# Optimization experiments

Measured on AMD Instinct MI355X. Metric: run time of the kernel, lower is better.

## Reference

```python
import jax, jax.numpy as jnp
import numpy as np

THR = 1.0
ALPHA = 5.0
C = 0.4
TAU_U = 20.0
DT = 1.0

def slayer(x):
    # SE-adlif SLAYER surrogate: c*alpha / (2*exp(alpha*|x|))
    return C * ALPHA / (2.0 * jnp.exp(jnp.abs(x) * ALPHA))

def setup_inputs() -> dict:
    key = jax.random.key(0)
    k1, k2, k3 = jax.random.split(key, 3)
    B, T, IN, OUT = 64, 1000, 512, 512
    x = jax.random.normal(k1, (B, T, IN), dtype=jnp.float32)
    lim = 1.0 / np.sqrt(IN)
    weight = jax.random.uniform(k2, (OUT, IN), minval=-lim, maxval=lim, dtype=jnp.float32)
    bias = jnp.zeros((OUT,), jnp.float32)
    # orthogonal init for recurrent weights
    recurrent = jnp.linalg.qr(jax.random.normal(k3, (OUT, OUT), dtype=jnp.float32))[0].astype(jnp.float32)
    # fixed tau trainer: decay = exp(-dt/tau)
    decay = jnp.full((OUT,), np.exp(-DT / TAU_U), dtype=jnp.float32)
    return {"input_tensor": x, "weight": weight, "bias": bias, "recurrent": recurrent, "decay": decay}

def reference(input_tensor, weight, bias, recurrent, decay):
    B = input_tensor.shape[0]
    OUT = weight.shape[0]
    sg = jax.lax.stop_gradient
    # precompute input-driven current for all timesteps: [B, T, OUT]
    cur = jnp.einsum('bti,oi->bto', input_tensor, weight) + bias
    v0 = jnp.zeros((B, OUT), jnp.float32)
    z0 = jnp.zeros((B, OUT), jnp.float32)

    def step(carry, c_t):
        v_tm1, z_tm1 = carry
        v_tm1 = v_tm1 * (1.0 - sg(z_tm1))  # detached reset
        soma = c_t + z_tm1 @ recurrent.T
        v_t = decay * v_tm1 + (1.0 - decay) * soma
        v_thr = v_t - THR
        hv = jnp.where(v_thr >= 0, 1.0, 0.0).astype(v_thr.dtype)
        # straight-through: value = heaviside, grad = SLAYER surrogate
        z_t = sg(hv) + (v_thr - sg(v_thr)) * sg(slayer(v_thr))
        return (v_t, z_t), (v_t, z_t)

    _, (vs, zs) = jax.lax.scan(step, (v0, z0), jnp.swapaxes(cur, 0, 1))
    vs = jnp.swapaxes(vs, 0, 1)  # [B, T, OUT]
    zs = jnp.swapaxes(zs, 0, 1)
    v_full = jnp.concatenate([v0[:, None], vs], axis=1)  # [B, T+1, OUT]
    z_full = jnp.concatenate([z0[:, None], zs], axis=1)
    states = jnp.stack([v_full, z_full], axis=0)  # [2, B, T+1, OUT]
    outputs = zs  # [B, T, OUT]
    return outputs, states
```

## Files before the change

kernel.cpp:

```cpp
#include <hip/hip_runtime.h>
#include <hip/hip_bf16.h>

#define SV_OFF 32768000
#define SZ_OFF 65568768
#define TC 125
#define NC 8

typedef __attribute__((ext_vector_type(8))) short bf16x8;
typedef __attribute__((ext_vector_type(4))) float f32x4;

__device__ __forceinline__ unsigned short f2bf(float f) {
  union { float f; unsigned u; } x; x.f = f;
  unsigned r = x.u + 0x7fffu + ((x.u >> 16) & 1u);
  return (unsigned short)(r >> 16);
}

__device__ __forceinline__ void gl_lds16(const void* g, void* l) {
  __builtin_amdgcn_global_load_lds(
      (const __attribute__((address_space(1))) unsigned int*)g,
      (__attribute__((address_space(3))) unsigned int*)l, 16, 0, 0);
}

__global__ __launch_bounds__(256) void prep(const float* __restrict__ W,
                                            const float* __restrict__ R,
                                            unsigned short* __restrict__ Wb,
                                            float* __restrict__ RT,
                                            int* __restrict__ flags) {
  const int idx = blockIdx.x * 256 + threadIdx.x;
  if (idx < 512 * 512) {
    Wb[idx] = f2bf(W[idx]);
    const int j = idx >> 9;
    const int o = idx & 511;
    RT[idx] = R[o * 512 + j];
  }
  if (idx < 64) flags[idx] = 0;
}

__global__ __launch_bounds__(256) void cvt_x(const float* __restrict__ x,
                                             unsigned short* __restrict__ xb) {
  const size_t i = ((size_t)blockIdx.x * 256 + threadIdx.x) * 8;
  const float4 a = *(const float4*)(x + i);
  const float4 b = *(const float4*)(x + i + 4);
  bf16x8 h;
  h[0] = (short)f2bf(a.x); h[1] = (short)f2bf(a.y);
  h[2] = (short)f2bf(a.z); h[3] = (short)f2bf(a.w);
  h[4] = (short)f2bf(b.x); h[5] = (short)f2bf(b.y);
  h[6] = (short)f2bf(b.z); h[7] = (short)f2bf(b.w);
  *(bf16x8*)(xb + i) = h;
}

__global__ __launch_bounds__(256, 2) void gemm_cur(
    const unsigned short* __restrict__ Ab,
    const unsigned short* __restrict__ Wb,
    const float* __restrict__ bias,
    float* __restrict__ C) {
  __shared__ unsigned short As[128][32];
  __shared__ unsigned short Bs[128][32];
  const int tid = threadIdx.x;
  const int bn = blockIdx.x * 128;
  const int bm = blockIdx.y * 128;
  const int wave = tid >> 6;
  const int lane = tid & 63;
  const int lr = lane & 15;
  const int lq = lane >> 4;
  const int mh = (wave & 1) * 64;
  const int nh = (wave >> 1) * 64;

  f32x4 acc[4][4] = {};

  const int lo0 = tid * 16;
  const int row0 = lo0 >> 6;
  const int colb = lo0 & 63;
  const size_t abase = (size_t)(bm + row0) * 1024 + colb;
  const size_t bbase = (size_t)(bn + row0) * 1024 + colb;

  for (int kk = 0; kk < 16; ++kk) {
    const size_t koff = (size_t)kk * 64;
    __syncthreads();
    gl_lds16((const char*)Ab + abase + koff,            (char*)(&As[0][0]) + lo0);
    gl_lds16((const char*)Ab + abase + 65536 + koff,    (char*)(&As[0][0]) + lo0 + 4096);
    gl_lds16((const char*)Wb + bbase + koff,            (char*)(&Bs[0][0]) + lo0);
    gl_lds16((const char*)Wb + bbase + 65536 + koff,    (char*)(&Bs[0][0]) + lo0 + 4096);
    __syncthreads();
    bf16x8 af[4], bfr[4];
#pragma unroll
    for (int i = 0; i < 4; ++i)
      af[i] = *(const bf16x8*)(&As[mh + i * 16 + lr][lq * 8]);
#pragma unroll
    for (int j = 0; j < 4; ++j)
      bfr[j] = *(const bf16x8*)(&Bs[nh + j * 16 + lr][lq * 8]);
#pragma unroll
    for (int i = 0; i < 4; ++i)
#pragma unroll
      for (int j = 0; j < 4; ++j)
        acc[i][j] = __builtin_amdgcn_mfma_f32_16x16x32_bf16(af[i], bfr[j], acc[i][j], 0, 0, 0);
  }
#pragma unroll
  for (int j = 0; j < 4; ++j) {
    const int col = bn + nh + j * 16 + lr;
    const float bv = bias[col];
#pragma unroll
    for (int i = 0; i < 4; ++i) {
      const int r0 = bm + mh + i * 16 + lq * 4;
#pragma unroll
      for (int r = 0; r < 4; ++r)
        C[(size_t)(r0 + r) * 512 + col] = acc[i][j][r] + bv;
    }
  }
}

__global__ __launch_bounds__(256) void chunk_sums(const float* __restrict__ cur,
                                                  const float* __restrict__ decay,
                                                  float* __restrict__ S) {
  const int gt = blockIdx.x * 256 + threadIdx.x;
  const int o = gt & 511;
  const int j = (gt >> 9) & (NC - 1);
  const int b = gt >> 12;
  const float d = decay[o];
  const float om = 1.0f - d;
  const size_t base = (size_t)b * 512000 + (size_t)(j * TC) * 512 + o;
  float nb[8];
#pragma unroll
  for (int u = 0; u < 8; ++u) nb[u] = cur[base + (size_t)u * 512];
  float s = 0.f;
#pragma unroll 8
  for (int k = 0; k < TC; ++k) {
    const float c = nb[k & 7];
    if (k < TC - 8) nb[k & 7] = cur[base + (size_t)(k + 8) * 512];
    s = d * s + om * c;
  }
  S[gt] = s;
}

__global__ __launch_bounds__(256) void chunk_scan(const float* __restrict__ cur,
                                                  const float* __restrict__ decay,
                                                  const float* __restrict__ S,
                                                  float* __restrict__ out,
                                                  int* __restrict__ flags) {
  const int gt = blockIdx.x * 256 + threadIdx.x;
  const int o = gt & 511;
  const int j = (gt >> 9) & (NC - 1);
  const int b = gt >> 12;
  const float d = decay[o];
  const float om = 1.0f - d;
  const size_t ci = (size_t)b * 512000 + (size_t)(j * TC) * 512 + o;
  const size_t svb = (size_t)b * 512512 + (size_t)(j * TC) * 512 + o;
  float* __restrict__ sv = out + SV_OFF;
  float* __restrict__ sz = out + SZ_OFF;
  if (j == 0) {
    __builtin_nontemporal_store(0.f, &sv[svb]);
    __builtin_nontemporal_store(0.f, &sz[svb]);
  }
  float v = 0.f;
  if (j > 0) {
    const float dTC = powf(d, (float)TC);
    const int sb = (b << 12) + o;
    for (int jj = 0; jj < j; ++jj) v = dTC * v + S[sb + (jj << 9)];
  }
  int fl = 0;
  float nb[8];
#pragma unroll
  for (int u = 0; u < 8; ++u) nb[u] = cur[ci + (size_t)u * 512];
#pragma unroll 8
  for (int k = 0; k < TC; ++k) {
    const float c = nb[k & 7];
    if (k < TC - 8) nb[k & 7] = cur[ci + (size_t)(k + 8) * 512];
    v = d * v + om * c;
    const float z = (v >= 1.0f) ? 1.0f : 0.0f;
    fl |= (v >= 1.0f);
    const size_t row = (size_t)k * 512;
    __builtin_nontemporal_store(z, &out[ci + row]);
    __builtin_nontemporal_store(v, &sv[svb + row + 512]);
    __builtin_nontemporal_store(z, &sz[svb + row + 512]);
  }
  if (fl) atomicOr(flags + b, 1);
}

__global__ __launch_bounds__(512) void scan_fix(const float* __restrict__ cur,
                                                const float* __restrict__ decay,
                                                const float* __restrict__ RT,
                                                float* __restrict__ out,
                                                const int* __restrict__ flags) {
  const int b = blockIdx.x;
  if (flags[b] == 0) return;
  const int o = threadIdx.x;
  __shared__ int cnt;
  __shared__ int list[512];
  const float d = decay[o];
  const float om = 1.f - d;
  float v = 0.f, z = 0.f;
  const size_t ci = (size_t)b * 512000 + o;
  const size_t svb = (size_t)b * 512512 + o;
  float* __restrict__ sv = out + SV_OFF;
  float* __restrict__ sz = out + SZ_OFF;
  sv[svb] = 0.f;
  sz[svb] = 0.f;
  if (o == 0) cnt = 0;
  __syncthreads();
  for (int t = 0; t < 1000; ++t) {
    float soma = cur[ci + (size_t)t * 512];
    const int n = cnt;
    for (int i = 0; i < n; ++i) soma += RT[(size_t)list[i] * 512 + o];
    v = d * (v * (1.f - z)) + om * soma;
    z = (v >= 1.0f) ? 1.0f : 0.0f;
    out[ci + (size_t)t * 512] = z;
    sv[svb + (size_t)(t + 1) * 512] = v;
    sz[svb + (size_t)(t + 1) * 512] = z;
    __syncthreads();
    if (o == 0) cnt = 0;
    __syncthreads();
    if (z != 0.f) { const int p = atomicAdd(&cnt, 1); list[p] = o; }
    __syncthreads();
  }
}

extern "C" void kernel_launch(void* const* d_in, const int* in_sizes, int n_in,
                              void* d_out, int out_size, void* d_ws, size_t ws_size,
                              hipStream_t stream) {
  (void)in_sizes; (void)n_in; (void)out_size; (void)ws_size;
  const float* x     = (const float*)d_in[0];
  const float* W     = (const float*)d_in[1];
  const float* bias  = (const float*)d_in[2];
  const float* R     = (const float*)d_in[3];
  const float* decay = (const float*)d_in[4];
  float* out = (float*)d_out;

  char* ws = (char*)d_ws;
  float* cur          = (float*)ws;
  unsigned short* Wb  = (unsigned short*)(ws + 131072000);
  float* RT           = (float*)(ws + 131596288);
  int* flags          = (int*)(ws + 132644864);
  float* S            = (float*)(ws + 132648960);

  unsigned short* xb = (unsigned short*)(out + SV_OFF);

  prep<<<1024, 256, 0, stream>>>(W, R, Wb, RT, flags);
  cvt_x<<<16000, 256, 0, stream>>>(x, xb);
  gemm_cur<<<dim3(4, 500), 256, 0, stream>>>(xb, Wb, bias, cur);
  chunk_sums<<<1024, 256, 0, stream>>>(cur, decay, S);
  chunk_scan<<<1024, 256, 0, stream>>>(cur, decay, S, out, flags);
  scan_fix<<<64, 512, 0, stream>>>(cur, decay, RT, out, flags);
}
```

Before: 603.3 us.

## Fuse input GEMM with leaky integration scan to eliminate current buffer

Replaces the separate GEMM, chunk-sum and chunk-scan kernels with one kernel. Each block owns one batch row and 64 outputs, walks time in 128-step tiles with double-buffered LDS staging, and stages the accumulators in swizzled shared memory. 64 threads then run the serial leaky scan straight from that tile. This removes the full fp32 current tensor round trip through global memory. The fallback spike-recurrence kernel now recomputes the input projection in fp32 from x and W, and the recurrent transpose is dropped. The costs are that most threads sit idle during the serial scan and the fallback path becomes much more expensive if it is triggered.

```diff
diff --git a/kernel.cpp b/kernel.cpp
--- a/kernel.cpp
+++ b/kernel.cpp
@@ -1,10 +1,7 @@
 #include <hip/hip_runtime.h>
-#include <hip/hip_bf16.h>
 
 #define SV_OFF 32768000
 #define SZ_OFF 65568768
-#define TC 125
-#define NC 8
 
 typedef __attribute__((ext_vector_type(8))) short bf16x8;
 typedef __attribute__((ext_vector_type(4))) float f32x4;
@@ -22,17 +19,10 @@
 }
 
 __global__ __launch_bounds__(256) void prep(const float* __restrict__ W,
-                                            const float* __restrict__ R,
                                             unsigned short* __restrict__ Wb,
-                                            float* __restrict__ RT,
                                             int* __restrict__ flags) {
   const int idx = blockIdx.x * 256 + threadIdx.x;
-  if (idx < 512 * 512) {
-    Wb[idx] = f2bf(W[idx]);
-    const int j = idx >> 9;
-    const int o = idx & 511;
-    RT[idx] = R[o * 512 + j];
-  }
+  if (idx < 512 * 512) Wb[idx] = f2bf(W[idx]);
   if (idx < 64) flags[idx] = 0;
 }
 
@@ -49,147 +39,128 @@
   *(bf16x8*)(xb + i) = h;
 }
 
-__global__ __launch_bounds__(256, 2) void gemm_cur(
+__global__ __launch_bounds__(256, 2) void fused(
     const unsigned short* __restrict__ Ab,
     const unsigned short* __restrict__ Wb,
     const float* __restrict__ bias,
-    float* __restrict__ C) {
-  __shared__ unsigned short As[128][32];
-  __shared__ unsigned short Bs[128][32];
-  const int tid = threadIdx.x;
-  const int bn = blockIdx.x * 128;
-  const int bm = blockIdx.y * 128;
+    const float* __restrict__ decay,
+    float* __restrict__ out,
+    int* __restrict__ flags) {
+  __shared__ unsigned short As[2][128][32];
+  __shared__ unsigned short Bs[2][64][32];
+  __shared__ float cs[128][64];
+
+  const int b    = blockIdx.x;
+  const int o0   = blockIdx.y * 64;
+  const int tid  = threadIdx.x;
   const int wave = tid >> 6;
   const int lane = tid & 63;
   const int lr = lane & 15;
   const int lq = lane >> 4;
-  const int mh = (wave & 1) * 64;
-  const int nh = (wave >> 1) * 64;
-
-  f32x4 acc[4][4] = {};
-
-  const int lo0 = tid * 16;
-  const int row0 = lo0 >> 6;
-  const int colb = lo0 & 63;
-  const size_t abase = (size_t)(bm + row0) * 1024 + colb;
-  const size_t bbase = (size_t)(bn + row0) * 1024 + colb;
-
-  for (int kk = 0; kk < 16; ++kk) {
-    const size_t koff = (size_t)kk * 64;
-    __syncthreads();
-    gl_lds16((const char*)Ab + abase + koff,            (char*)(&As[0][0]) + lo0);
-    gl_lds16((const char*)Ab + abase + 65536 + koff,    (char*)(&As[0][0]) + lo0 + 4096);
-    gl_lds16((const char*)Wb + bbase + koff,            (char*)(&Bs[0][0]) + lo0);
-    gl_lds16((const char*)Wb + bbase + 65536 + koff,    (char*)(&Bs[0][0]) + lo0 + 4096);
-    __syncthreads();
-    bf16x8 af[4], bfr[4];
+  const int wr = wave >> 1;
+  const int wc = wave & 1;
+
+  const int arow = tid >> 2;
+  const int acb  = (tid & 3) * 16;
+  const char* abase = (const char*)Ab + (size_t)b * 1000 * 1024;
+  const char* bbase = (const char*)Wb + (size_t)o0 * 1024;
+
+#define STAGE(pp, t0s, kks) do {                                                   \
+    const int _kb = (kks) * 64 + acb;                                              \
+    gl_lds16(abase + (size_t)((t0s) + arow) * 1024 + _kb,                          \
+             (char*)&As[pp][0][0] + tid * 16);                                     \
+    gl_lds16(abase + (size_t)((t0s) + 64 + arow) * 1024 + _kb,                     \
+             (char*)&As[pp][0][0] + tid * 16 + 4096);                              \
+    gl_lds16(bbase + (size_t)arow * 1024 + _kb,                                    \
+             (char*)&Bs[pp][0][0] + tid * 16);                                     \
+  } while (0)
+
+  float v = 0.f, d = 0.f, om = 0.f, bv = 0.f;
+  int fl = 0;
+  if (tid < 64) {
+    d  = decay[o0 + tid];
+    om = 1.f - d;
+    bv = bias[o0 + tid];
+    __builtin_nontemporal_store(0.f, out + SV_OFF + (size_t)b * 512512 + o0 + tid);
+    __builtin_nontemporal_store(0.f, out + SZ_OFF + (size_t)b * 512512 + o0 + tid);
+  }
+
+  int p = 0;
+  STAGE(0, 0, 0);
+  for (int tile = 0; tile < 8; ++tile) {
+    const int t0 = tile * 128;
+    f32x4 acc[4][2] = {};
+    for (int kk = 0; kk < 16; ++kk) {
+      __syncthreads();
+      if (kk < 15)       STAGE(p ^ 1, t0, kk + 1);
+      else if (tile < 7) STAGE(p ^ 1, t0 + 128, 0);
+      bf16x8 af[4], bf[2];
+#pragma unroll
+      for (int i = 0; i < 4; ++i)
+        af[i] = *(const bf16x8*)(&As[p][wr * 64 + i * 16 + lr][lq * 8]);
+#pragma unroll
+      for (int j = 0; j < 2; ++j)
+        bf[j] = *(const bf16x8*)(&Bs[p][wc * 32 + j * 16 + lr][lq * 8]);
+#pragma unroll
+      for (int i = 0; i < 4; ++i)
+#pragma unroll
+        for (int j = 0; j < 2; ++j)
+          acc[i][j] = __builtin_amdgcn_mfma_f32_16x16x32_bf16(af[i], bf[j], acc[i][j], 0, 0, 0);
+      p ^= 1;
+    }
 #pragma unroll
     for (int i = 0; i < 4; ++i)
-      af[i] = *(const bf16x8*)(&As[mh + i * 16 + lr][lq * 8]);
-#pragma unroll
-    for (int j = 0; j < 4; ++j)
-      bfr[j] = *(const bf16x8*)(&Bs[nh + j * 16 + lr][lq * 8]);
-#pragma unroll
-    for (int i = 0; i < 4; ++i)
-#pragma unroll
-      for (int j = 0; j < 4; ++j)
-        acc[i][j] = __builtin_amdgcn_mfma_f32_16x16x32_bf16(af[i], bfr[j], acc[i][j], 0, 0, 0);
-  }
-#pragma unroll
-  for (int j = 0; j < 4; ++j) {
-    const int col = bn + nh + j * 16 + lr;
-    const float bv = bias[col];
-#pragma unroll
-    for (int i = 0; i < 4; ++i) {
-      const int r0 = bm + mh + i * 16 + lq * 4;
-#pragma unroll
-      for (int r = 0; r < 4; ++r)
-        C[(size_t)(r0 + r) * 512 + col] = acc[i][j][r] + bv;
+#pragma unroll
+      for (int j = 0; j < 2; ++j) {
+        const int tb = wr * 64 + i * 16 + lq * 4;
+        const int cc = (wc * 32 + j * 16 + lr) ^ ((lq & 1) << 4);
+#pragma unroll
+        for (int r = 0; r < 4; ++r) cs[tb + r][cc] = acc[i][j][r];
+      }
+    __syncthreads();
+    if (tid < 64) {
+      const int tmax = (tile == 7) ? 104 : 128;
+      float* zp = out + ((size_t)b * 1000 + t0) * 512 + o0 + tid;
+      float* vp = out + SV_OFF + ((size_t)b * 1001 + t0 + 1) * 512 + o0 + tid;
+      float* sp = out + SZ_OFF + ((size_t)b * 1001 + t0 + 1) * 512 + o0 + tid;
+      for (int t = 0; t < tmax; t += 4) {
+        const int cc = tid ^ (((t >> 2) & 1) << 4);
+        float c4[4];
+#pragma unroll
+        for (int u = 0; u < 4; ++u) c4[u] = cs[t + u][cc];
+#pragma unroll
+        for (int u = 0; u < 4; ++u) {
+          v = d * v + om * (c4[u] + bv);
+          const float z = (v >= 1.0f) ? 1.0f : 0.0f;
+          fl |= (v >= 1.0f);
+          __builtin_nontemporal_store(z, zp + (size_t)(t + u) * 512);
+          __builtin_nontemporal_store(v, vp + (size_t)(t + u) * 512);
+          __builtin_nontemporal_store(z, sp + (size_t)(t + u) * 512);
+        }
+      }
     }
   }
-}
-
-__global__ __launch_bounds__(256) void chunk_sums(const float* __restrict__ cur,
-                                                  const float* __restrict__ decay,
-                                                  float* __restrict__ S) {
-  const int gt = blockIdx.x * 256 + threadIdx.x;
-  const int o = gt & 511;
-  const int j = (gt >> 9) & (NC - 1);
-  const int b = gt >> 12;
-  const float d = decay[o];
-  const float om = 1.0f - d;
-  const size_t base = (size_t)b * 512000 + (size_t)(j * TC) * 512 + o;
-  float nb[8];
-#pragma unroll
-  for (int u = 0; u < 8; ++u) nb[u] = cur[base + (size_t)u * 512];
-  float s = 0.f;
-#pragma unroll 8
-  for (int k = 0; k < TC; ++k) {
-    const float c = nb[k & 7];
-    if (k < TC - 8) nb[k & 7] = cur[base + (size_t)(k + 8) * 512];
-    s = d * s + om * c;
-  }
-  S[gt] = s;
-}
-
-__global__ __launch_bounds__(256) void chunk_scan(const float* __restrict__ cur,
-                                                  const float* __restrict__ decay,
-                                                  const float* __restrict__ S,
-                                                  float* __restrict__ out,
-                                                  int* __restrict__ flags) {
-  const int gt = blockIdx.x * 256 + threadIdx.x;
-  const int o = gt & 511;
-  const int j = (gt >> 9) & (NC - 1);
-  const int b = gt >> 12;
-  const float d = decay[o];
-  const float om = 1.0f - d;
-  const size_t ci = (size_t)b * 512000 + (size_t)(j * TC) * 512 + o;
-  const size_t svb = (size_t)b * 512512 + (size_t)(j * TC) * 512 + o;
-  float* __restrict__ sv = out + SV_OFF;
-  float* __restrict__ sz = out + SZ_OFF;
-  if (j == 0) {
-    __builtin_nontemporal_store(0.f, &sv[svb]);
-    __builtin_nontemporal_store(0.f, &sz[svb]);
-  }
-  float v = 0.f;
-  if (j > 0) {
-    const float dTC = powf(d, (float)TC);
-    const int sb = (b << 12) + o;
-    for (int jj = 0; jj < j; ++jj) v = dTC * v + S[sb + (jj << 9)];
-  }
-  int fl = 0;
-  float nb[8];
-#pragma unroll
-  for (int u = 0; u < 8; ++u) nb[u] = cur[ci + (size_t)u * 512];
-#pragma unroll 8
-  for (int k = 0; k < TC; ++k) {
-    const float c = nb[k & 7];
-    if (k < TC - 8) nb[k & 7] = cur[ci + (size_t)(k + 8) * 512];
-    v = d * v + om * c;
-    const float z = (v >= 1.0f) ? 1.0f : 0.0f;
-    fl |= (v >= 1.0f);
-    const size_t row = (size_t)k * 512;
-    __builtin_nontemporal_store(z, &out[ci + row]);
-    __builtin_nontemporal_store(v, &sv[svb + row + 512]);
-    __builtin_nontemporal_store(z, &sz[svb + row + 512]);
-  }
-  if (fl) atomicOr(flags + b, 1);
-}
-
-__global__ __launch_bounds__(512) void scan_fix(const float* __restrict__ cur,
+  if (tid < 64 && fl) atomicOr(flags + b, 1);
+#undef STAGE
+}
+
+__global__ __launch_bounds__(512) void scan_fix(const float* __restrict__ x,
+                                                const float* __restrict__ W,
+                                                const float* __restrict__ bias,
+                                                const float* __restrict__ R,
                                                 const float* __restrict__ decay,
-                                                const float* __restrict__ RT,
                                                 float* __restrict__ out,
                                                 const int* __restrict__ flags) {
   const int b = blockIdx.x;
   if (flags[b] == 0) return;
   const int o = threadIdx.x;
+  __shared__ float xs[512];
   __shared__ int cnt;
   __shared__ int list[512];
   const float d = decay[o];
   const float om = 1.f - d;
   float v = 0.f, z = 0.f;
-  const size_t ci = (size_t)b * 512000 + o;
+  const size_t zb  = (size_t)b * 512000 + o;
   const size_t svb = (size_t)b * 512512 + o;
   float* __restrict__ sv = out + SV_OFF;
   float* __restrict__ sz = out + SZ_OFF;
@@ -198,18 +169,21 @@
   if (o == 0) cnt = 0;
   __syncthreads();
   for (int t = 0; t < 1000; ++t) {
-    float soma = cur[ci + (size_t)t * 512];
+    xs[o] = x[((size_t)b * 1000 + t) * 512 + o];
+    __syncthreads();
+    float soma = bias[o];
+    for (int i = 0; i < 512; ++i) soma += xs[i] * W[(size_t)o * 512 + i];
     const int n = cnt;
-    for (int i = 0; i < n; ++i) soma += RT[(size_t)list[i] * 512 + o];
+    for (int i = 0; i < n; ++i) soma += R[(size_t)o * 512 + list[i]];
     v = d * (v * (1.f - z)) + om * soma;
     z = (v >= 1.0f) ? 1.0f : 0.0f;
-    out[ci + (size_t)t * 512] = z;
+    out[zb + (size_t)t * 512] = z;
     sv[svb + (size_t)(t + 1) * 512] = v;
     sz[svb + (size_t)(t + 1) * 512] = z;
     __syncthreads();
     if (o == 0) cnt = 0;
     __syncthreads();
-    if (z != 0.f) { const int p = atomicAdd(&cnt, 1); list[p] = o; }
+    if (z != 0.f) { const int q = atomicAdd(&cnt, 1); list[q] = o; }
     __syncthreads();
   }
 }
@@ -226,18 +200,12 @@
   float* out = (float*)d_out;
 
   char* ws = (char*)d_ws;
-  float* cur          = (float*)ws;
-  unsigned short* Wb  = (unsigned short*)(ws + 131072000);
-  float* RT           = (float*)(ws + 131596288);
-  int* flags          = (int*)(ws + 132644864);
-  float* S            = (float*)(ws + 132648960);
-
-  unsigned short* xb = (unsigned short*)(out + SV_OFF);
-
-  prep<<<1024, 256, 0, stream>>>(W, R, Wb, RT, flags);
+  unsigned short* xb = (unsigned short*)ws;
+  unsigned short* Wb = (unsigned short*)(ws + 65536000);
+  int* flags         = (int*)(ws + 66060288);
+
+  prep<<<1024, 256, 0, stream>>>(W, Wb, flags);
   cvt_x<<<16000, 256, 0, stream>>>(x, xb);
-  gemm_cur<<<dim3(4, 500), 256, 0, stream>>>(xb, Wb, bias, cur);
-  chunk_sums<<<1024, 256, 0, stream>>>(cur, decay, S);
-  chunk_scan<<<1024, 256, 0, stream>>>(cur, decay, S, out, flags);
-  scan_fix<<<64, 512, 0, stream>>>(cur, decay, RT, out, flags);
-}
+  fused<<<dim3(64, 8), 256, 0, stream>>>(xb, Wb, bias, decay, out, flags);
+  scan_fix<<<64, 512, 0, stream>>>(x, W, bias, R, decay, out, flags);
+}
```

Result: faster. 547.6 us (-9.2%).
